# Kernel tuning notes

Measured on AMD Instinct MI355X. Metric: run time of the kernel, lower is better.

The kernel has to match this reference:

```python
import jax, jax.numpy as jnp
import numpy as np

K = 3  # kernel size, stride=1, padding=0 (hardcoded in SingleAdder)


def setup_inputs() -> dict:
    key = jax.random.key(0)
    x = jax.random.normal(key, (16, 5, 512, 512), dtype=jnp.float32)
    # adder weight is initialized to all-ones in SingleAdder.__init__
    W = jnp.ones((5, 5, 3, 3), dtype=jnp.float32)
    return {"x": x, "W": W}


def adder2d(x, W):
    """AdderNet conv: out[n,co,i,j] = -sum_{ci,kh,kw} |x[n,ci,i+kh,j+kw] - W[co,ci,kh,kw]|.
    Loop over the 9 fixed kernel taps (not data dims); each tap is fully vectorized.
    Avoids materializing a full im2col tensor."""
    B, Ci, H, Wd = x.shape
    Co = W.shape[0]
    Ho, Wo = H - K + 1, Wd - K + 1
    out = jnp.zeros((B, Co, Ho, Wo), dtype=x.dtype)
    for kh in range(K):
        for kw in range(K):
            patch = x[:, None, :, kh:kh + Ho, kw:kw + Wo]        # [B,1,Ci,Ho,Wo]
            w = W[None, :, :, kh, kw, None, None]                # [1,Co,Ci,1,1]
            out = out - jnp.sum(jnp.abs(patch - w), axis=2)      # reduce over Ci
    return out


def reference(x, W):
    return adder2d(x, W)
```

## Files before the change

### kernel.cpp

```cpp
#include <hip/hip_runtime.h>


#define KK 3
#define NB 16
#define CI 5
#define CO 5
#define H 512
#define WD 512
#define HO 510
#define WO 510
#define TW 64
#define TH 16

__global__ __launch_bounds__(256)
void adder2d_kernel(const float* __restrict__ x,
                    const float* __restrict__ Wg,
                    float* __restrict__ out) {
    const int tx = threadIdx.x & 63;
    const int ty = threadIdx.x >> 6;
    const int j0 = blockIdx.x * TW;
    const int i0 = blockIdx.y * TH;
    const int n  = blockIdx.z;

    const int j     = j0 + tx;
    const int ibase = i0 + ty * 4;

    float xv[CI][6][KK];
    const float* xn = x + (size_t)n * CI * H * WD;
    #pragma unroll
    for (int ci = 0; ci < CI; ++ci) {
        #pragma unroll
        for (int r = 0; r < 6; ++r) {
            int gi = ibase + r;
            gi = gi < H ? gi : H - 1;
            const float* rowp = xn + (size_t)ci * H * WD + (size_t)gi * WD;
            #pragma unroll
            for (int k = 0; k < KK; ++k) {
                int gj = j + k;
                gj = gj < WD ? gj : WD - 1;
                xv[ci][r][k] = rowp[gj];
            }
        }
    }

    const bool jvalid = (j < WO);
    float* outn = out + (size_t)n * CO * HO * WO;

    #pragma unroll 1
    for (int co = 0; co < CO; ++co) {
        float acc0 = 0.f, acc1 = 0.f, acc2 = 0.f, acc3 = 0.f;
        const float* wp = Wg + co * (CI * KK * KK);
        #pragma unroll
        for (int ci = 0; ci < CI; ++ci) {
            #pragma unroll
            for (int kh = 0; kh < KK; ++kh) {
                #pragma unroll
                for (int kw = 0; kw < KK; ++kw) {
                    const float w = wp[ci * 9 + kh * 3 + kw];
                    acc0 += fabsf(xv[ci][kh + 0][kw] - w);
                    acc1 += fabsf(xv[ci][kh + 1][kw] - w);
                    acc2 += fabsf(xv[ci][kh + 2][kw] - w);
                    acc3 += fabsf(xv[ci][kh + 3][kw] - w);
                }
            }
        }
        if (jvalid) {
            float accs[4] = {acc0, acc1, acc2, acc3};
            float* outc = outn + (size_t)co * HO * WO;
            #pragma unroll
            for (int rr = 0; rr < 4; ++rr) {
                const int i = ibase + rr;
                if (i < HO) outc[(size_t)i * WO + j] = -accs[rr];
            }
        }
    }
}

extern "C" void kernel_launch(void* const* d_in, const int* in_sizes, int n_in,
                              void* d_out, int out_size, void* d_ws, size_t ws_size,
                              hipStream_t stream) {
    const float* x  = (const float*)d_in[0];
    const float* Wg = (const float*)d_in[1];
    float* out      = (float*)d_out;

    dim3 grid((WO + TW - 1) / TW,
              (HO + TH - 1) / TH,
              NB);
    dim3 block(256);
    adder2d_kernel<<<grid, block, 0, stream>>>(x, Wg, out);
}
```

Measured before the change: 157.3 us.

## Swap loop order to stream input channels with per-output accumulators

```diff
diff --git a/kernel.cpp b/kernel.cpp
--- a/kernel.cpp
+++ b/kernel.cpp
@@ -25,52 +25,58 @@
     const int j     = j0 + tx;
     const int ibase = i0 + ty * 4;
 
-    float xv[CI][6][KK];
+    int gi[6];
+    #pragma unroll
+    for (int r = 0; r < 6; ++r) { int v = ibase + r; gi[r] = v < H ? v : H - 1; }
+    int gj[KK];
+    #pragma unroll
+    for (int k = 0; k < KK; ++k) { int v = j + k; gj[k] = v < WD ? v : WD - 1; }
+
+    float acc[CO][4];
+    #pragma unroll
+    for (int co = 0; co < CO; ++co)
+        #pragma unroll
+        for (int r = 0; r < 4; ++r) acc[co][r] = 0.f;
+
     const float* xn = x + (size_t)n * CI * H * WD;
+
     #pragma unroll
     for (int ci = 0; ci < CI; ++ci) {
+        float xv[6][KK];
+        const float* xc = xn + (size_t)ci * H * WD;
         #pragma unroll
         for (int r = 0; r < 6; ++r) {
-            int gi = ibase + r;
-            gi = gi < H ? gi : H - 1;
-            const float* rowp = xn + (size_t)ci * H * WD + (size_t)gi * WD;
+            const float* rowp = xc + (size_t)gi[r] * WD;
             #pragma unroll
-            for (int k = 0; k < KK; ++k) {
-                int gj = j + k;
-                gj = gj < WD ? gj : WD - 1;
-                xv[ci][r][k] = rowp[gj];
+            for (int k = 0; k < KK; ++k) xv[r][k] = rowp[gj[k]];
+        }
+
+        #pragma unroll
+        for (int co = 0; co < CO; ++co) {
+            const float* wp = Wg + (co * CI + ci) * (KK * KK);
+            #pragma unroll
+            for (int kh = 0; kh < KK; ++kh) {
+                #pragma unroll
+                for (int kw = 0; kw < KK; ++kw) {
+                    const float w = wp[kh * 3 + kw];
+                    acc[co][0] += fabsf(xv[kh + 0][kw] - w);
+                    acc[co][1] += fabsf(xv[kh + 1][kw] - w);
+                    acc[co][2] += fabsf(xv[kh + 2][kw] - w);
+                    acc[co][3] += fabsf(xv[kh + 3][kw] - w);
+                }
             }
         }
     }
 
-    const bool jvalid = (j < WO);
-    float* outn = out + (size_t)n * CO * HO * WO;
-
-    #pragma unroll 1
-    for (int co = 0; co < CO; ++co) {
-        float acc0 = 0.f, acc1 = 0.f, acc2 = 0.f, acc3 = 0.f;
-        const float* wp = Wg + co * (CI * KK * KK);
+    if (j < WO) {
+        float* outn = out + (size_t)n * CO * HO * WO;
         #pragma unroll
-        for (int ci = 0; ci < CI; ++ci) {
-            #pragma unroll
-            for (int kh = 0; kh < KK; ++kh) {
-                #pragma unroll
-                for (int kw = 0; kw < KK; ++kw) {
-                    const float w = wp[ci * 9 + kh * 3 + kw];
-                    acc0 += fabsf(xv[ci][kh + 0][kw] - w);
-                    acc1 += fabsf(xv[ci][kh + 1][kw] - w);
-                    acc2 += fabsf(xv[ci][kh + 2][kw] - w);
-                    acc3 += fabsf(xv[ci][kh + 3][kw] - w);
-                }
-            }
-        }
-        if (jvalid) {
-            float accs[4] = {acc0, acc1, acc2, acc3};
+        for (int co = 0; co < CO; ++co) {
             float* outc = outn + (size_t)co * HO * WO;
             #pragma unroll
             for (int rr = 0; rr < 4; ++rr) {
                 const int i = ibase + rr;
-                if (i < HO) outc[(size_t)i * WO + j] = -accs[rr];
+                if (i < HO) outc[(size_t)i * WO + j] = -acc[co][rr];
             }
         }
     }
```

Result: slower. 166.7 us (+5.9%).
